# Kernel tuning notes

Hardware: AMD Instinct MI355X
Metric: run time of the kernel (lower is better)

## Reference

```python
import jax, jax.numpy as jnp
import numpy as np

W_LEN = 37  # window_length
EPS = 1e-9
LRELU_SLOPE = 0.2
SQRT2 = 1.4142135623730951


def win_sum(x, w):
    # Depthwise sliding-window sum of width w, 'same' padding w//2 (odd w).
    # Equivalent to the diag-kernel conv1d in the original code, but O(T) via cumsum.
    pad = w // 2
    xp = jnp.pad(x, ((0, 0), (0, 0), (pad, pad)))
    cs = jnp.cumsum(xp, axis=-1)
    cs = jnp.pad(cs, ((0, 0), (0, 0), (1, 0)))
    return cs[..., w:] - cs[..., :-w]


def conv1d(x, w, b):
    # x: [B,C,T], w: [O,I,3], padding=1
    y = jax.lax.conv_general_dilated(x, w, (1,), [(1, 1)],
                                     dimension_numbers=('NCH', 'OIH', 'NCH'))
    return y + b[None, :, None]


def adawin_instance(x, s, mask, fc_w, fc_b, alpha):
    # x: [B,C,T], s: [B,S,T], mask: [B,T]
    C = x.shape[1]
    h = jnp.einsum('bst,cs->bct', s, fc_w) + fc_b[None, :, None]  # [B,2C,T]
    m = mask[:, None, :]                       # [B,1,T]
    denom = win_sum(m, W_LEN) + EPS            # same for all channels
    gamma = win_sum(h[:, :C], W_LEN) / denom * m
    beta = win_sum(h[:, C:], W_LEN) / denom * m
    x_norm = jnp.tanh(alpha * x)               # WindowedNorm1d.forward
    return (1.0 + gamma) * x_norm + beta


def setup_inputs() -> dict:
    key = jax.random.key(0)
    ks = jax.random.split(key, 10)
    B, C_IN, C_OUT, S, T = 16, 512, 512, 128, 2048
    inp = {
        'x': jax.random.normal(ks[0], (B, C_IN, T), dtype=jnp.float32),
        's': jax.random.normal(ks[1], (B, S, T), dtype=jnp.float32),
        'lengths': jax.random.randint(ks[2], (B,), 0, T).astype(jnp.int32),
        'fc1_w': jax.random.normal(ks[3], (2 * C_IN, S), dtype=jnp.float32) * 0.05,
        'fc1_b': jnp.zeros((2 * C_IN,), dtype=jnp.float32),
        'alpha1': jnp.full((1,), 0.5, dtype=jnp.float32),
        'conv1_w': jax.random.normal(ks[4], (C_OUT, C_IN, 3), dtype=jnp.float32) * 0.02,
        'conv1_b': jnp.zeros((C_OUT,), dtype=jnp.float32),
        'fc2_w': jax.random.normal(ks[5], (2 * C_OUT, S), dtype=jnp.float32) * 0.05,
        'fc2_b': jnp.zeros((2 * C_OUT,), dtype=jnp.float32),
        'alpha2': jnp.full((1,), 0.5, dtype=jnp.float32),
        'conv2_w': jax.random.normal(ks[6], (C_OUT, C_OUT, 3), dtype=jnp.float32) * 0.02,
        'conv2_b': jnp.zeros((C_OUT,), dtype=jnp.float32),
    }
    return inp


def reference(x, s, lengths, fc1_w, fc1_b, alpha1, conv1_w, conv1_b,
              fc2_w, fc2_b, alpha2, conv2_w, conv2_b):
    T = x.shape[2]
    mask = (jnp.arange(T)[None, :] < lengths[:, None]).astype(x.dtype)  # [B,T]

    h = adawin_instance(x, s, mask, fc1_w, fc1_b, alpha1)
    h = jax.nn.leaky_relu(h, LRELU_SLOPE)
    h = conv1d(h, conv1_w, conv1_b)
    h = adawin_instance(h, s, mask, fc2_w, fc2_b, alpha2)
    h = jax.nn.leaky_relu(h, LRELU_SLOPE)
    h = conv1d(h, conv2_w, conv2_b)

    # dim_in == dim_out -> identity shortcut
    return (h + x) / SQRT2
```

## Files before the change

kernel.cpp:

```cpp
#include <hip/hip_runtime.h>

#define B_ 16
#define C_ 512
#define S_ 128
#define T_ 2048
#define HALF 18
#define WLEN 37

typedef __bf16 bf16x8 __attribute__((ext_vector_type(8)));
typedef float f32x4 __attribute__((ext_vector_type(4)));
typedef float f32x16 __attribute__((ext_vector_type(16)));
typedef unsigned short ushort_t;

__device__ inline ushort_t f2bf(float x) {
    unsigned u = __float_as_uint(x);
    u += 0x7fffu + ((u >> 16) & 1u);
    return (ushort_t)(u >> 16);
}
__device__ inline float bf2f(ushort_t h) {
    return __uint_as_float(((unsigned)h) << 16);
}
__device__ inline float fast_tanh(float z) {
    float e = __expf(2.f * z);
    return 1.f - __fdividef(2.f, e + 1.f);
}
__device__ __forceinline__ void glds16(const void* g, void* l) {
    __builtin_amdgcn_global_load_lds(
        (const __attribute__((address_space(1))) unsigned*)g,
        (__attribute__((address_space(3))) unsigned*)l, 16, 0, 0);
}

#define MFMA16(a, b, c) __builtin_amdgcn_mfma_f32_16x16x32_bf16((a), (b), (c), 0, 0, 0)
#define MFMA32(a, b, c) __builtin_amdgcn_mfma_f32_32x32x16_bf16((a), (b), (c), 0, 0, 0)

__global__ void prep_weights(const float* __restrict__ fc1, const float* __restrict__ fc2,
                             ushort_t* __restrict__ Wfc) {
    const int n_fc = 1024 * 128;
    int idx = blockIdx.x * blockDim.x + threadIdx.x;
    if (idx < n_fc) Wfc[idx] = f2bf(fc1[idx]);
    else if (idx < 2 * n_fc) Wfc[idx] = f2bf(fc2[idx - n_fc]);
}

__global__ void prep_conv_images(const float* __restrict__ c1, const float* __restrict__ c2,
                                 ushort_t* __restrict__ I1, ushort_t* __restrict__ I2) {
    int idx = blockIdx.x * blockDim.x + threadIdx.x;
    const int per_conv = 4 * 16 * 1664;
    if (idx >= 2 * per_conv) return;
    int conv = idx >= per_conv;
    int rr = conv ? idx - per_conv : idx;
    const float* src = conv ? c2 : c1;
    ushort_t* dst = conv ? I2 : I1;
    int blkch = rr / 1664;
    int G = rr - blkch * 1664;
    int r = G / 13;
    int g = G - r * 13;
    ushort_t vals[8];
    if (g == 12) {
#pragma unroll
        for (int e = 0; e < 8; ++e) vals[e] = 0;
    } else {
        int tap = g >> 2, seg = g & 3;
        int o = (blkch >> 4) * 128 + r;
        int chb = (blkch & 15) * 32 + seg * 8;
#pragma unroll
        for (int e = 0; e < 8; ++e)
            vals[e] = f2bf(src[(size_t)(o * 512 + chb + e) * 3 + tap]);
    }
    uint4 pk;
    pk.x = vals[0] | ((unsigned)vals[1] << 16);
    pk.y = vals[2] | ((unsigned)vals[3] << 16);
    pk.z = vals[4] | ((unsigned)vals[5] << 16);
    pk.w = vals[6] | ((unsigned)vals[7] << 16);
    *(uint4*)&dst[(size_t)rr * 8] = pk;
}

__global__ void zero_pads(ushort_t* __restrict__ y1p, ushort_t* __restrict__ y2p) {
    int tid = blockIdx.x * blockDim.x + threadIdx.x;
    if (tid < 4096) {
        ushort_t* base = (tid & 1) ? y2p : y1p;
        int r = tid >> 1;
        int bb = r >> 7;
        int rowsel = (r >> 6) & 1;
        int col = (r & 63) * 8;
        size_t row = (size_t)bb * (T_ + 2) + (rowsel ? (T_ + 1) : 0);
        *(uint4*)&base[row * C_ + col] = (uint4){0, 0, 0, 0};
    }
}

__global__ __launch_bounds__(256) void winsum_kernel(const float* __restrict__ s,
                                                     ushort_t* __restrict__ sw_t) {
    int b = blockIdx.y;
    int t0 = blockIdx.x * 64;
    __shared__ float sb[128][101];
    int tid = threadIdx.x;
    for (int e = tid; e < 128 * 100; e += 256) {
        int sj = e / 100;
        int u = e - sj * 100;
        int gt = t0 - HALF + u;
        float v = 0.f;
        if (gt >= 0 && gt < T_) v = s[((size_t)(b * S_ + sj)) * T_ + gt];
        sb[sj][u] = v;
    }
    __syncthreads();
    for (int e = tid; e < 64 * 128; e += 256) {
        int tl = e >> 7;
        int sj = e & 127;
        float sum = 0.f;
#pragma unroll
        for (int d = 0; d < WLEN; ++d) sum += sb[sj][tl + d];
        sw_t[((size_t)(b * T_ + t0 + tl)) * S_ + sj] = f2bf(sum);
    }
}

template <int INLAYOUT>
__global__ __launch_bounds__(256) void adawin_kernel(
    const void* __restrict__ xin_, const ushort_t* __restrict__ sw_t,
    const ushort_t* __restrict__ Wfc, const float* __restrict__ fcb,
    const float* __restrict__ alpha, const int* __restrict__ lengths,
    ushort_t* __restrict__ youtp) {
    int t0 = blockIdx.x * 64;
    int c0 = blockIdx.y * 64;
    int b = blockIdx.z;
    __shared__ __attribute__((aligned(16))) ushort_t smem[128 * 136 + 64 * 136];
    ushort_t (*As)[136] = (ushort_t(*)[136])smem;
    ushort_t (*Bs)[136] = (ushort_t(*)[136])(smem + 128 * 136);
    int tid = threadIdx.x;

    {
        int r = tid >> 4;
        int cseg = (tid & 15) * 8;
#pragma unroll
        for (int p = 0; p < 8; ++p) {
            int row = p * 16 + r;
            int grow = (row < 64) ? (c0 + row) : (448 + c0 + row);
            *(uint4*)&As[row][cseg] = *(const uint4*)&Wfc[(size_t)grow * 128 + cseg];
        }
    }
    {
        int tl = tid & 63;
        int sg = tid >> 6;
        const ushort_t* src = &sw_t[((size_t)(b * T_ + t0 + tl)) * S_];
#pragma unroll
        for (int j = 0; j < 4; ++j) {
            int col = sg * 32 + j * 8;
            *(uint4*)&Bs[tl][col] = *(const uint4*)&src[col];
        }
    }
    __syncthreads();

    int wave = tid >> 6, lane = tid & 63;
    int quad = lane >> 4, l = lane & 15;
    f32x4 accg[4], accb[4];
#pragma unroll
    for (int n = 0; n < 4; ++n) {
        accg[n] = (f32x4){0.f, 0.f, 0.f, 0.f};
        accb[n] = (f32x4){0.f, 0.f, 0.f, 0.f};
    }
    int rg = wave * 16 + l;
    int rb = 64 + wave * 16 + l;
#pragma unroll
    for (int ks = 0; ks < 4; ++ks) {
        int kc = ks * 32 + quad * 8;
        bf16x8 ag = *(const bf16x8*)&As[rg][kc];
        bf16x8 ab = *(const bf16x8*)&As[rb][kc];
#pragma unroll
        for (int n = 0; n < 4; ++n) {
            bf16x8 bb = *(const bf16x8*)&Bs[n * 16 + l][kc];
            accg[n] = MFMA16(ag, bb, accg[n]);
            accb[n] = MFMA16(ab, bb, accb[n]);
        }
    }

    __syncthreads();
    ushort_t (*Ts)[72] = (ushort_t(*)[72])smem;

    int len = lengths[b];
    float alph = alpha[0];
    const float* xf = (const float*)xin_;
    const ushort_t* xh = (const ushort_t*)xin_;
    int clocal = wave * 16 + quad * 4;
    int cbase = c0 + clocal;
#pragma unroll
    for (int n = 0; n < 4; ++n) {
        int t = t0 + n * 16 + l;
        int lo = t - HALF; if (lo < 0) lo = 0;
        int hi = t + HALF; if (hi > T_ - 1) hi = T_ - 1;
        float cnt = (float)(hi - lo + 1);
        int hv = hi < (len - 1) ? hi : (len - 1);
        int mdi = hv - lo + 1; if (mdi < 0) mdi = 0;
        float m = (t < len) ? 1.f : 0.f;
        float sc = m / ((float)mdi + 1e-9f);

        float xv[4];
        if (INLAYOUT == 0) {
#pragma unroll
            for (int j = 0; j < 4; ++j)
                xv[j] = xf[(size_t)(b * C_ + cbase + j) * T_ + t];
        } else {
            uint2 xraw = *(const uint2*)&xh[((size_t)(b * (T_ + 2) + 1 + t)) * C_ + cbase];
            xv[0] = bf2f((ushort_t)(xraw.x & 0xffff));
            xv[1] = bf2f((ushort_t)(xraw.x >> 16));
            xv[2] = bf2f((ushort_t)(xraw.y & 0xffff));
            xv[3] = bf2f((ushort_t)(xraw.y >> 16));
        }
        unsigned pk[2];
#pragma unroll
        for (int j = 0; j < 4; ++j) {
            int c = cbase + j;
            float gamma = (accg[n][j] + fcb[c] * cnt) * sc;
            float beta = (accb[n][j] + fcb[C_ + c] * cnt) * sc;
            float xn = fast_tanh(alph * xv[j]);
            float v = (1.f + gamma) * xn + beta;
            v = v > 0.f ? v : 0.2f * v;
            unsigned hv16 = (unsigned)f2bf(v);
            if (j & 1) pk[j >> 1] |= hv16 << 16;
            else pk[j >> 1] = hv16;
        }
        *(uint2*)&Ts[n * 16 + l][clocal] = (uint2){pk[0], pk[1]};
    }
    __syncthreads();
    {
        int row = tid >> 2;
        int seg = (tid & 3) * 16;
        size_t gbase = ((size_t)(b * (T_ + 2) + 1 + t0 + row)) * C_ + c0 + seg;
        *(uint4*)&youtp[gbase] = *(const uint4*)&Ts[row][seg];
        *(uint4*)&youtp[gbase + 8] = *(const uint4*)&Ts[row][seg + 8];
    }
}

#define A_BYTES 26624
#define B_BYTES 11264
__device__ __forceinline__ void conv_stage(const char* aimg, const char* xt, int ch,
                                           char* Ab, char* Bb, int wave, int lane) {
#pragma unroll
    for (int i = 0; i < 37; ++i) {
        if ((i & 3) != wave) continue;
        if (i < 26) {
            glds16(aimg + i * 1024 + lane * 16, Ab + i * 1024);
        } else {
            int j = i - 26;
            int gi = j * 64 + lane;
            int r = gi / 5;
            int gg = gi - r * 5;
            if (gg == 4) gg = 0;
            glds16(xt + (size_t)r * 1024 + ch * 64 + gg * 16, Bb + j * 1024);
        }
    }
}

template <int EPI>
__global__ __launch_bounds__(256) void conv_kernel(
    const ushort_t* __restrict__ Xp, const ushort_t* __restrict__ Wimg,
    const float* __restrict__ bias, const float* __restrict__ resid,
    ushort_t* __restrict__ out_bf, float* __restrict__ out_f) {
    int t0 = blockIdx.x * 128;
    int o0 = blockIdx.y * 128;
    int b = blockIdx.z;
    __shared__ __attribute__((aligned(16))) char smembuf[2 * A_BYTES + 2 * B_BYTES];
    int tid = threadIdx.x;
    int lane = tid & 63, wave = tid >> 6;
    int l32 = lane & 31, khalf = lane >> 5;
    int wo = (wave & 1) * 64, wt = (wave >> 1) * 64;

    const char* imgbase = (const char*)Wimg + (size_t)blockIdx.y * 16 * A_BYTES;
    const char* xt = (const char*)Xp + (size_t)(b * (T_ + 2) + t0) * 1024;

    f32x16 acc[2][2];
#pragma unroll
    for (int io = 0; io < 2; ++io)
#pragma unroll
        for (int it = 0; it < 2; ++it)
#pragma unroll
            for (int r = 0; r < 16; ++r) acc[io][it][r] = 0.f;

    conv_stage(imgbase, xt, 0, smembuf, smembuf + 2 * A_BYTES, wave, lane);
    asm volatile("s_waitcnt vmcnt(0)" ::: "memory");
    __syncthreads();

#pragma unroll 1
    for (int ch = 0; ch < 16; ++ch) {
        int cur = ch & 1;
        if (ch < 15)
            conv_stage(imgbase + (size_t)(ch + 1) * A_BYTES, xt, ch + 1,
                       smembuf + (cur ^ 1) * A_BYTES,
                       smembuf + 2 * A_BYTES + (cur ^ 1) * B_BYTES, wave, lane);
        ushort_t (*As)[104] = (ushort_t(*)[104])(smembuf + cur * A_BYTES);
        ushort_t (*Bs)[40] = (ushort_t(*)[40])(smembuf + 2 * A_BYTES + cur * B_BYTES);
#pragma unroll
        for (int tap = 0; tap < 3; ++tap) {
#pragma unroll
            for (int ks = 0; ks < 2; ++ks) {
                int kc = tap * 32 + ks * 16 + khalf * 8;
                bf16x8 a0 = *(const bf16x8*)&As[wo + l32][kc];
                bf16x8 a1 = *(const bf16x8*)&As[wo + 32 + l32][kc];
#pragma unroll
                for (int it = 0; it < 2; ++it) {
                    bf16x8 bb =
                        *(const bf16x8*)&Bs[wt + it * 32 + l32 + tap][ks * 16 + khalf * 8];
                    acc[0][it] = MFMA32(a0, bb, acc[0][it]);
                    acc[1][it] = MFMA32(a1, bb, acc[1][it]);
                }
            }
        }
        asm volatile("s_waitcnt vmcnt(0)" ::: "memory");
        __syncthreads();
    }

    if (EPI == 0) {
        ushort_t (*Ts)[136] = (ushort_t(*)[136])smembuf;
#pragma unroll
        for (int io = 0; io < 2; ++io)
#pragma unroll
            for (int it = 0; it < 2; ++it) {
                int trow = wt + it * 32 + l32;
#pragma unroll
                for (int g = 0; g < 4; ++g) {
                    int oc = wo + io * 32 + g * 8 + khalf * 4;
                    unsigned pk[2];
#pragma unroll
                    for (int j = 0; j < 4; ++j) {
                        float v = acc[io][it][g * 4 + j] + bias[o0 + oc + j];
                        unsigned hv16 = (unsigned)f2bf(v);
                        if (j & 1) pk[j >> 1] |= hv16 << 16;
                        else pk[j >> 1] = hv16;
                    }
                    *(uint2*)&Ts[trow][oc] = (uint2){pk[0], pk[1]};
                }
            }
        __syncthreads();
        int cc = (tid & 15) * 8;
        int rbse = tid >> 4;
#pragma unroll
        for (int j = 0; j < 8; ++j) {
            int row = j * 16 + rbse;
            *(uint4*)&out_bf[((size_t)(b * (T_ + 2) + 1 + t0 + row)) * C_ + o0 + cc] =
                *(const uint4*)&Ts[row][cc];
        }
    } else {
#pragma unroll
        for (int io = 0; io < 2; ++io)
#pragma unroll
            for (int it = 0; it < 2; ++it) {
                int obase = o0 + wo + io * 32;
                int t = t0 + wt + it * 32 + l32;
#pragma unroll
                for (int g = 0; g < 4; ++g) {
                    int oo = obase + g * 8 + khalf * 4;
#pragma unroll
                    for (int j = 0; j < 4; ++j) {
                        size_t off = (size_t)(b * C_ + oo + j) * T_ + t;
                        out_f[off] = (acc[io][it][g * 4 + j] + bias[oo + j] + resid[off]) *
                                     0.70710678118654752f;
                    }
                }
            }
    }
}

extern "C" void kernel_launch(void* const* d_in, const int* in_sizes, int n_in,
                              void* d_out, int out_size, void* d_ws, size_t ws_size,
                              hipStream_t stream) {
    const float* x = (const float*)d_in[0];
    const float* s = (const float*)d_in[1];
    const int* lengths = (const int*)d_in[2];
    const float* fc1_w = (const float*)d_in[3];
    const float* fc1_b = (const float*)d_in[4];
    const float* alpha1 = (const float*)d_in[5];
    const float* conv1_w = (const float*)d_in[6];
    const float* conv1_b = (const float*)d_in[7];
    const float* fc2_w = (const float*)d_in[8];
    const float* fc2_b = (const float*)d_in[9];
    const float* alpha2 = (const float*)d_in[10];
    const float* conv2_w = (const float*)d_in[11];
    const float* conv2_b = (const float*)d_in[12];

    const size_t IMG = (size_t)4 * 16 * 1664 * 8;
    char* ws = (char*)d_ws;
    ushort_t* sw_t = (ushort_t*)ws; ws += (size_t)B_ * T_ * S_ * 2;
    ushort_t* Wfc = (ushort_t*)ws;  ws += (size_t)2 * 1024 * 128 * 2;
    ushort_t* I1 = (ushort_t*)ws;   ws += IMG * 2;
    ushort_t* I2 = (ushort_t*)ws;   ws += IMG * 2;
    ushort_t* y2p = (ushort_t*)ws;  ws += (size_t)B_ * (T_ + 2) * C_ * 2;
    ushort_t* y1p = (ushort_t*)ws;  ws += (size_t)B_ * (T_ + 2) * C_ * 2;
    ws += 12 * 1024;
    if ((size_t)(ws - (char*)d_ws) > ws_size) return;

    prep_weights<<<dim3(1024), dim3(256), 0, stream>>>(fc1_w, fc2_w, Wfc);
    prep_conv_images<<<dim3(832), dim3(256), 0, stream>>>(conv1_w, conv2_w, I1, I2);
    winsum_kernel<<<dim3(32, 16), dim3(256), 0, stream>>>(s, sw_t);
    zero_pads<<<dim3(16), dim3(256), 0, stream>>>(y1p, y2p);
    adawin_kernel<0><<<dim3(32, 8, 16), dim3(256), 0, stream>>>(
        (const void*)x, sw_t, Wfc, fc1_b, alpha1, lengths, y1p);
    conv_kernel<0><<<dim3(16, 4, 16), dim3(256), 0, stream>>>(
        y1p, I1, conv1_b, (const float*)nullptr, y2p, (float*)nullptr);
    adawin_kernel<1><<<dim3(32, 8, 16), dim3(256), 0, stream>>>(
        (const void*)y2p, sw_t, Wfc + 1024 * 128, fc2_b, alpha2, lengths, y1p);
    conv_kernel<1><<<dim3(16, 4, 16), dim3(256), 0, stream>>>(
        y1p, I2, conv2_b, x, (ushort_t*)nullptr, (float*)d_out);
}
```

Measured before the change: 362.3 us.

## Widen conv tiles to 256 time steps with 8 waves and triple-buffered B staging

The conv kernel now covers 256 time steps per block using 512 threads (8 waves). A-fragments are held in registers and reused across two time sub-tiles. B (activation) tiles rotate through a triple buffer, and the global-to-LDS loads use partial vmcnt waits with barriers, so loading the next channel chunk overlaps MFMA work. MFMA phases also raise wave priority. The weight image is padded to 28 KB per chunk to match the new staging layout. The trade-off is larger LDS use and more register pressure, which may limit occupancy.

Result: slower. 382.4 us (+5.6%).

```diff
diff --git a/kernel.cpp b/kernel.cpp
--- a/kernel.cpp
+++ b/kernel.cpp
@@ -41,30 +41,37 @@
     else if (idx < 2 * n_fc) Wfc[idx] = f2bf(fc2[idx - n_fc]);
 }
 
+#define A_BYTES 28672
+#define B_BYTES 12288
 __global__ void prep_conv_images(const float* __restrict__ c1, const float* __restrict__ c2,
                                  ushort_t* __restrict__ I1, ushort_t* __restrict__ I2) {
     int idx = blockIdx.x * blockDim.x + threadIdx.x;
-    const int per_conv = 4 * 16 * 1664;
+    const int per_conv = 4 * 16 * 1792;
     if (idx >= 2 * per_conv) return;
     int conv = idx >= per_conv;
     int rr = conv ? idx - per_conv : idx;
     const float* src = conv ? c2 : c1;
     ushort_t* dst = conv ? I2 : I1;
-    int blkch = rr / 1664;
-    int G = rr - blkch * 1664;
-    int r = G / 13;
-    int g = G - r * 13;
+    int blkch = rr / 1792;
+    int G = rr - blkch * 1792;
     ushort_t vals[8];
-    if (g == 12) {
+    if (G >= 1664) {
 #pragma unroll
         for (int e = 0; e < 8; ++e) vals[e] = 0;
     } else {
-        int tap = g >> 2, seg = g & 3;
-        int o = (blkch >> 4) * 128 + r;
-        int chb = (blkch & 15) * 32 + seg * 8;
-#pragma unroll
-        for (int e = 0; e < 8; ++e)
-            vals[e] = f2bf(src[(size_t)(o * 512 + chb + e) * 3 + tap]);
+        int r = G / 13;
+        int g = G - r * 13;
+        if (g == 12) {
+#pragma unroll
+            for (int e = 0; e < 8; ++e) vals[e] = 0;
+        } else {
+            int tap = g >> 2, seg = g & 3;
+            int o = (blkch >> 4) * 128 + r;
+            int chb = (blkch & 15) * 32 + seg * 8;
+#pragma unroll
+            for (int e = 0; e < 8; ++e)
+                vals[e] = f2bf(src[(size_t)(o * 512 + chb + e) * 3 + tap]);
+        }
     }
     uint4 pk;
     pk.x = vals[0] | ((unsigned)vals[1] << 16);
@@ -228,39 +235,51 @@
     }
 }
 
-#define A_BYTES 26624
-#define B_BYTES 11264
-__device__ __forceinline__ void conv_stage(const char* aimg, const char* xt, int ch,
+__device__ __forceinline__ void stage_full(const char* img, const char* xts_ch,
                                            char* Ab, char* Bb, int wave, int lane) {
 #pragma unroll
-    for (int i = 0; i < 37; ++i) {
-        if ((i & 3) != wave) continue;
-        if (i < 26) {
-            glds16(aimg + i * 1024 + lane * 16, Ab + i * 1024);
+    for (int i = 0; i < 40; ++i) {
+        if ((i & 7) != wave) continue;
+        if (i < 28) {
+            glds16(img + i * 1024 + lane * 16, Ab + i * 1024);
         } else {
-            int j = i - 26;
+            int j = i - 28;
             int gi = j * 64 + lane;
             int r = gi / 5;
             int gg = gi - r * 5;
             if (gg == 4) gg = 0;
-            glds16(xt + (size_t)r * 1024 + ch * 64 + gg * 16, Bb + j * 1024);
-        }
+            if (r > 129) r = 129;
+            glds16(xts_ch + (size_t)r * 1024 + gg * 16, Bb + j * 1024);
+        }
+    }
+}
+__device__ __forceinline__ void stage_b(const char* xts_ch, char* Bb, int wave, int lane) {
+#pragma unroll
+    for (int j = 0; j < 12; ++j) {
+        if ((j & 7) != wave) continue;
+        int gi = j * 64 + lane;
+        int r = gi / 5;
+        int gg = gi - r * 5;
+        if (gg == 4) gg = 0;
+        if (r > 129) r = 129;
+        glds16(xts_ch + (size_t)r * 1024 + gg * 16, Bb + j * 1024);
     }
 }
 
 template <int EPI>
-__global__ __launch_bounds__(256) void conv_kernel(
+__global__ __launch_bounds__(512, 2) void conv_kernel(
     const ushort_t* __restrict__ Xp, const ushort_t* __restrict__ Wimg,
     const float* __restrict__ bias, const float* __restrict__ resid,
     ushort_t* __restrict__ out_bf, float* __restrict__ out_f) {
-    int t0 = blockIdx.x * 128;
+    int t0 = blockIdx.x * 256;
     int o0 = blockIdx.y * 128;
     int b = blockIdx.z;
-    __shared__ __attribute__((aligned(16))) char smembuf[2 * A_BYTES + 2 * B_BYTES];
+    __shared__ __attribute__((aligned(16))) char smembuf[2 * A_BYTES + 3 * B_BYTES];
+    char* Bbase = smembuf + 2 * A_BYTES;
     int tid = threadIdx.x;
     int lane = tid & 63, wave = tid >> 6;
     int l32 = lane & 31, khalf = lane >> 5;
-    int wo = (wave & 1) * 64, wt = (wave >> 1) * 64;
+    int wo = (wave & 1) * 64, wt = (wave >> 1) * 32;
 
     const char* imgbase = (const char*)Wimg + (size_t)blockIdx.y * 16 * A_BYTES;
     const char* xt = (const char*)Xp + (size_t)(b * (T_ + 2) + t0) * 1024;
@@ -269,57 +288,86 @@
 #pragma unroll
     for (int io = 0; io < 2; ++io)
 #pragma unroll
-        for (int it = 0; it < 2; ++it)
-#pragma unroll
-            for (int r = 0; r < 16; ++r) acc[io][it][r] = 0.f;
-
-    conv_stage(imgbase, xt, 0, smembuf, smembuf + 2 * A_BYTES, wave, lane);
-    asm volatile("s_waitcnt vmcnt(0)" ::: "memory");
-    __syncthreads();
-
+        for (int ts = 0; ts < 2; ++ts)
+#pragma unroll
+            for (int r = 0; r < 16; ++r) acc[io][ts][r] = 0.f;
+
+    stage_full(imgbase, xt, smembuf, Bbase, wave, lane);
+    stage_b(xt + 131072, Bbase + B_BYTES, wave, lane);
+
+    int bc = 0;
 #pragma unroll 1
     for (int ch = 0; ch < 16; ++ch) {
-        int cur = ch & 1;
+        char* Acur = smembuf + (ch & 1) * A_BYTES;
+        char* Anxt = smembuf + ((ch & 1) ^ 1) * A_BYTES;
+        int bc1 = bc + 1; if (bc1 >= 3) bc1 -= 3;
+        int bc2 = bc + 2; if (bc2 >= 3) bc2 -= 3;
+
+        asm volatile("s_waitcnt vmcnt(1)\ns_barrier" ::: "memory");
         if (ch < 15)
-            conv_stage(imgbase + (size_t)(ch + 1) * A_BYTES, xt, ch + 1,
-                       smembuf + (cur ^ 1) * A_BYTES,
-                       smembuf + 2 * A_BYTES + (cur ^ 1) * B_BYTES, wave, lane);
-        ushort_t (*As)[104] = (ushort_t(*)[104])(smembuf + cur * A_BYTES);
-        ushort_t (*Bs)[40] = (ushort_t(*)[40])(smembuf + 2 * A_BYTES + cur * B_BYTES);
-#pragma unroll
-        for (int tap = 0; tap < 3; ++tap) {
+            stage_full(imgbase + (size_t)(ch + 1) * A_BYTES, xt + (size_t)(ch + 1) * 64,
+                       Anxt, Bbase + bc2 * B_BYTES, wave, lane);
+        ushort_t (*As)[104] = (ushort_t(*)[104])Acur;
+        bf16x8 a[3][2][2];
+#pragma unroll
+        for (int tap = 0; tap < 3; ++tap)
 #pragma unroll
             for (int ks = 0; ks < 2; ++ks) {
                 int kc = tap * 32 + ks * 16 + khalf * 8;
-                bf16x8 a0 = *(const bf16x8*)&As[wo + l32][kc];
-                bf16x8 a1 = *(const bf16x8*)&As[wo + 32 + l32][kc];
-#pragma unroll
-                for (int it = 0; it < 2; ++it) {
-                    bf16x8 bb =
-                        *(const bf16x8*)&Bs[wt + it * 32 + l32 + tap][ks * 16 + khalf * 8];
-                    acc[0][it] = MFMA32(a0, bb, acc[0][it]);
-                    acc[1][it] = MFMA32(a1, bb, acc[1][it]);
+                a[tap][ks][0] = *(const bf16x8*)&As[wo + l32][kc];
+                a[tap][ks][1] = *(const bf16x8*)&As[wo + 32 + l32][kc];
+            }
+        {
+            ushort_t (*Bs)[40] = (ushort_t(*)[40])(Bbase + bc * B_BYTES);
+            __builtin_amdgcn_s_setprio(1);
+#pragma unroll
+            for (int tap = 0; tap < 3; ++tap)
+#pragma unroll
+                for (int ks = 0; ks < 2; ++ks) {
+                    bf16x8 bb = *(const bf16x8*)&Bs[wt + l32 + tap][ks * 16 + khalf * 8];
+                    acc[0][0] = MFMA32(a[tap][ks][0], bb, acc[0][0]);
+                    acc[1][0] = MFMA32(a[tap][ks][1], bb, acc[1][0]);
                 }
-            }
-        }
-        asm volatile("s_waitcnt vmcnt(0)" ::: "memory");
+            __builtin_amdgcn_s_setprio(0);
+        }
+
+        if (ch < 15) {
+            asm volatile("s_waitcnt vmcnt(5)\ns_barrier" ::: "memory");
+            stage_b(xt + 131072 + (size_t)(ch + 1) * 64, Bbase + bc * B_BYTES, wave, lane);
+        } else {
+            asm volatile("s_waitcnt vmcnt(0)\ns_barrier" ::: "memory");
+        }
+        {
+            ushort_t (*Bs)[40] = (ushort_t(*)[40])(Bbase + bc1 * B_BYTES);
+            __builtin_amdgcn_s_setprio(1);
+#pragma unroll
+            for (int tap = 0; tap < 3; ++tap)
+#pragma unroll
+                for (int ks = 0; ks < 2; ++ks) {
+                    bf16x8 bb = *(const bf16x8*)&Bs[wt + l32 + tap][ks * 16 + khalf * 8];
+                    acc[0][1] = MFMA32(a[tap][ks][0], bb, acc[0][1]);
+                    acc[1][1] = MFMA32(a[tap][ks][1], bb, acc[1][1]);
+                }
+            __builtin_amdgcn_s_setprio(0);
+        }
+        bc = bc2;
+    }
+
+    if (EPI == 0) {
         __syncthreads();
-    }
-
-    if (EPI == 0) {
         ushort_t (*Ts)[136] = (ushort_t(*)[136])smembuf;
 #pragma unroll
-        for (int io = 0; io < 2; ++io)
-#pragma unroll
-            for (int it = 0; it < 2; ++it) {
-                int trow = wt + it * 32 + l32;
+        for (int ts = 0; ts < 2; ++ts)
+#pragma unroll
+            for (int io = 0; io < 2; ++io) {
+                int trow = ts * 128 + wt + l32;
 #pragma unroll
                 for (int g = 0; g < 4; ++g) {
                     int oc = wo + io * 32 + g * 8 + khalf * 4;
                     unsigned pk[2];
 #pragma unroll
                     for (int j = 0; j < 4; ++j) {
-                        float v = acc[io][it][g * 4 + j] + bias[o0 + oc + j];
+                        float v = acc[io][ts][g * 4 + j] + bias[o0 + oc + j];
                         unsigned hv16 = (unsigned)f2bf(v);
                         if (j & 1) pk[j >> 1] |= hv16 << 16;
                         else pk[j >> 1] = hv16;
@@ -328,28 +376,25 @@
                 }
             }
         __syncthreads();
-        int cc = (tid & 15) * 8;
-        int rbse = tid >> 4;
-#pragma unroll
-        for (int j = 0; j < 8; ++j) {
-            int row = j * 16 + rbse;
-            *(uint4*)&out_bf[((size_t)(b * (T_ + 2) + 1 + t0 + row)) * C_ + o0 + cc] =
-                *(const uint4*)&Ts[row][cc];
-        }
+        int row = tid >> 1;
+        int segh = (tid & 1) * 64;
+        size_t gbase = ((size_t)(b * (T_ + 2) + 1 + t0 + row)) * C_ + o0 + segh;
+#pragma unroll
+        for (int j = 0; j < 8; ++j)
+            *(uint4*)&out_bf[gbase + j * 8] = *(const uint4*)&Ts[row][segh + j * 8];
     } else {
 #pragma unroll
         for (int io = 0; io < 2; ++io)
 #pragma unroll
-            for (int it = 0; it < 2; ++it) {
-                int obase = o0 + wo + io * 32;
-                int t = t0 + wt + it * 32 + l32;
+            for (int ts = 0; ts < 2; ++ts) {
+                int t = t0 + ts * 128 + wt + l32;
 #pragma unroll
                 for (int g = 0; g < 4; ++g) {
-                    int oo = obase + g * 8 + khalf * 4;
+                    int oo = o0 + wo + io * 32 + g * 8 + khalf * 4;
 #pragma unroll
                     for (int j = 0; j < 4; ++j) {
                         size_t off = (size_t)(b * C_ + oo + j) * T_ + t;
-                        out_f[off] = (acc[io][it][g * 4 + j] + bias[oo + j] + resid[off]) *
+                        out_f[off] = (acc[io][ts][g * 4 + j] + bias[oo + j] + resid[off]) *
                                      0.70710678118654752f;
                     }
                 }
@@ -374,27 +419,27 @@
     const float* conv2_w = (const float*)d_in[11];
     const float* conv2_b = (const float*)d_in[12];
 
-    const size_t IMG = (size_t)4 * 16 * 1664 * 8;
+    const size_t IMGB = (size_t)4 * 16 * A_BYTES;
     char* ws = (char*)d_ws;
     ushort_t* sw_t = (ushort_t*)ws; ws += (size_t)B_ * T_ * S_ * 2;
     ushort_t* Wfc = (ushort_t*)ws;  ws += (size_t)2 * 1024 * 128 * 2;
-    ushort_t* I1 = (ushort_t*)ws;   ws += IMG * 2;
-    ushort_t* I2 = (ushort_t*)ws;   ws += IMG * 2;
+    ushort_t* I1 = (ushort_t*)ws;   ws += IMGB;
+    ushort_t* I2 = (ushort_t*)ws;   ws += IMGB;
     ushort_t* y2p = (ushort_t*)ws;  ws += (size_t)B_ * (T_ + 2) * C_ * 2;
     ushort_t* y1p = (ushort_t*)ws;  ws += (size_t)B_ * (T_ + 2) * C_ * 2;
     ws += 12 * 1024;
     if ((size_t)(ws - (char*)d_ws) > ws_size) return;
 
     prep_weights<<<dim3(1024), dim3(256), 0, stream>>>(fc1_w, fc2_w, Wfc);
-    prep_conv_images<<<dim3(832), dim3(256), 0, stream>>>(conv1_w, conv2_w, I1, I2);
+    prep_conv_images<<<dim3(896), dim3(256), 0, stream>>>(conv1_w, conv2_w, I1, I2);
     winsum_kernel<<<dim3(32, 16), dim3(256), 0, stream>>>(s, sw_t);
     zero_pads<<<dim3(16), dim3(256), 0, stream>>>(y1p, y2p);
     adawin_kernel<0><<<dim3(32, 8, 16), dim3(256), 0, stream>>>(
         (const void*)x, sw_t, Wfc, fc1_b, alpha1, lengths, y1p);
-    conv_kernel<0><<<dim3(16, 4, 16), dim3(256), 0, stream>>>(
+    conv_kernel<0><<<dim3(8, 4, 16), dim3(512), 0, stream>>>(
         y1p, I1, conv1_b, (const float*)nullptr, y2p, (float*)nullptr);
     adawin_kernel<1><<<dim3(32, 8, 16), dim3(256), 0, stream>>>(
         (const void*)y2p, sw_t, Wfc + 1024 * 128, fc2_b, alpha2, lengths, y1p);
-    conv_kernel<1><<<dim3(16, 4, 16), dim3(256), 0, stream>>>(
+    conv_kernel<1><<<dim3(8, 4, 16), dim3(512), 0, stream>>>(
         y1p, I2, conv2_b, x, (ushort_t*)nullptr, (float*)d_out);
 }
```
